# Kernel tuning notes

Measured on AMD Instinct MI355X. Metric: run time of the kernel, lower is better.

Reference implementation:

```python
import jax, jax.numpy as jnp
import numpy as np

D_MODEL, D_STATE, DT_RANK = 1024, 16, 64
BATCH, SEQLEN = 2, 4096

def setup_inputs() -> dict:
    key = jax.random.key(0)
    ks = jax.random.split(key, 6)
    x = jax.random.normal(ks[0], (BATCH, SEQLEN, D_MODEL), dtype=jnp.float32)
    # A = arange(1..N) repeated per channel; A_log = log(A)
    A = jnp.tile(jnp.arange(1, D_STATE + 1, dtype=jnp.float32)[None, :], (D_MODEL, 1))
    A_log = jnp.log(A)
    D_param = jnp.ones((D_MODEL,), dtype=jnp.float32)
    dt_init_std = DT_RANK ** -0.5
    dt_proj_w = jax.random.uniform(ks[1], (D_MODEL, DT_RANK), minval=-dt_init_std, maxval=dt_init_std, dtype=jnp.float32)
    dt = jnp.exp(jax.random.uniform(ks[2], (D_MODEL,)) * (np.log(0.1) - np.log(0.001)) + np.log(0.001))
    dt_proj_b = dt + jnp.log(-jnp.expm1(-dt))
    x_to_dtBC_w = jax.random.normal(ks[3], (DT_RANK + 2 * D_STATE, D_MODEL), dtype=jnp.float32) * (D_MODEL ** -0.5)
    return {"x": x, "A_log": A_log, "D_param": D_param, "dt_proj_w": dt_proj_w, "dt_proj_b": dt_proj_b, "x_to_dtBC_w": x_to_dtBC_w}

def reference(x, A_log, D_param, dt_proj_w, dt_proj_b, x_to_dtBC_w):
    # x: (B,L,D)
    dtBC = jnp.einsum('bld,ed->ble', x, x_to_dtBC_w)            # (B,L,dt_rank+2N)
    dt_in = dtBC[..., :DT_RANK]
    B_in = dtBC[..., DT_RANK:DT_RANK + D_STATE]                  # (B,L,N)
    C_in = dtBC[..., DT_RANK + D_STATE:]                         # (B,L,N)
    dt = jax.nn.softplus(jnp.einsum('blr,dr->bld', dt_in, dt_proj_w) + dt_proj_b)  # (B,L,D)
    A = -jnp.exp(A_log)                                          # (D,N)
    dA = jnp.exp(dt[..., None] * A[None, None])                  # (B,L,D,N)
    dB = dt[..., None] * B_in[:, :, None, :]                     # (B,L,D,N)
    dBx = dB * x[..., None]                                      # (B,L,D,N)

    def step(h, inputs):
        dA_t, dBx_t, C_t = inputs                                # (B,D,N),(B,D,N),(B,N)
        h = dA_t * h + dBx_t
        y_t = jnp.einsum('bdn,bn->bd', h, C_t)
        return h, y_t

    h0 = jnp.zeros((x.shape[0], D_MODEL, D_STATE), dtype=x.dtype)
    xs = (jnp.swapaxes(dA, 0, 1), jnp.swapaxes(dBx, 0, 1), jnp.swapaxes(C_in, 0, 1))
    _, ys = jax.lax.scan(step, h0, xs)                           # (L,B,D)
    y = jnp.swapaxes(ys, 0, 1) + x * D_param[None, None, :]
    return y
```

## Files before the change

kernel.cpp:

```cpp
#include <hip/hip_runtime.h>

#define D_MODEL 1024
#define D_STATE 16
#define DT_RANK 64
#define BATCH 2
#define SEQLEN 4096
#define NROWS (BATCH * SEQLEN)
#define E_DIM (DT_RANK + 2 * D_STATE)
#define CH 32
#define NCH (SEQLEN / CH)

__global__ __launch_bounds__(256)
void k_trans(const float* __restrict__ Wx, const float* __restrict__ W2,
             float* __restrict__ WT, float* __restrict__ W2T) {
  const int bid = blockIdx.x;
  if (bid < 384) {
    const int idx = bid * 256 + threadIdx.x;
    const int k = idx / E_DIM;
    const int e = idx - k * E_DIM;
    WT[idx] = Wx[(size_t)e * D_MODEL + k];
  } else {
    const int idx = (bid - 384) * 256 + threadIdx.x;
    const int r = idx >> 10;
    const int d = idx & 1023;
    W2T[idx] = W2[(size_t)d * DT_RANK + r];
  }
}

#define G1_BM 64
#define KSPLIT 8
#define KSEG (D_MODEL / KSPLIT)

__global__ __launch_bounds__(128)
void k_gemm1(const float* __restrict__ x, const float* __restrict__ WT,
             float* __restrict__ parts) {
  __shared__ float sX[64 * 65];
  const int tid = threadIdx.x;
  const int lane = tid & 63;
  const int e0 = __builtin_amdgcn_readfirstlane((tid >> 6) * 48);
  const int m0 = blockIdx.x * G1_BM;
  const int ks0 = blockIdx.y * KSEG;

  float acc[48];
  #pragma unroll
  for (int j = 0; j < 48; ++j) acc[j] = 0.f;

  for (int kk = 0; kk < KSEG; kk += 64) {
    __syncthreads();
    #pragma unroll
    for (int s = 0; s < 8; ++s) {
      const int f = s * 128 + tid;
      const int r = f >> 4;
      const int k4 = f & 15;
      const float4 v = *reinterpret_cast<const float4*>(
          &x[(size_t)(m0 + r) * D_MODEL + ks0 + kk + k4 * 4]);
      sX[(k4 * 4 + 0) * 65 + r] = v.x;
      sX[(k4 * 4 + 1) * 65 + r] = v.y;
      sX[(k4 * 4 + 2) * 65 + r] = v.z;
      sX[(k4 * 4 + 3) * 65 + r] = v.w;
    }
    __syncthreads();
    #pragma unroll 4
    for (int k = 0; k < 64; ++k) {
      const float xv = sX[k * 65 + lane];
      const float* wrow = WT + (size_t)(ks0 + kk + k) * E_DIM + e0;
      #pragma unroll
      for (int q = 0; q < 12; ++q) {
        const float4 w = *reinterpret_cast<const float4*>(wrow + 4 * q);
        acc[4 * q + 0] = fmaf(xv, w.x, acc[4 * q + 0]);
        acc[4 * q + 1] = fmaf(xv, w.y, acc[4 * q + 1]);
        acc[4 * q + 2] = fmaf(xv, w.z, acc[4 * q + 2]);
        acc[4 * q + 3] = fmaf(xv, w.w, acc[4 * q + 3]);
      }
    }
  }
  float* op = parts + (size_t)blockIdx.y * (NROWS * E_DIM)
            + (size_t)(m0 + lane) * E_DIM + e0;
  #pragma unroll
  for (int q = 0; q < 12; ++q)
    *reinterpret_cast<float4*>(op + 4 * q) =
        make_float4(acc[4 * q + 0], acc[4 * q + 1], acc[4 * q + 2], acc[4 * q + 3]);
}

__global__ __launch_bounds__(256)
void k_reduce(const float* __restrict__ parts, float* __restrict__ dtBC) {
  const int i = blockIdx.x * 256 + threadIdx.x;
  const float4* p = reinterpret_cast<const float4*>(parts);
  float4 a = p[i];
  #pragma unroll
  for (int s = 1; s < KSPLIT; ++s) {
    const float4 b = p[(size_t)s * (NROWS * E_DIM / 4) + i];
    a.x += b.x; a.y += b.y; a.z += b.z; a.w += b.w;
  }
  reinterpret_cast<float4*>(dtBC)[i] = a;
}

#define G2_ROWS 16

__global__ __launch_bounds__(256)
void k_dt(const float* __restrict__ dtBC, const float* __restrict__ W2T,
          const float* __restrict__ b2, float* __restrict__ dt) {
  const int d = blockIdx.x * 256 + threadIdx.x;
  const int m0 = blockIdx.y * G2_ROWS;
  const float bias = b2[d];
  float acc[G2_ROWS];
  #pragma unroll
  for (int i = 0; i < G2_ROWS; ++i) acc[i] = bias;

  for (int r = 0; r < DT_RANK; ++r) {
    const float w = W2T[(size_t)r * D_MODEL + d];
    #pragma unroll
    for (int i = 0; i < G2_ROWS; ++i)
      acc[i] = fmaf(dtBC[(size_t)(m0 + i) * E_DIM + r], w, acc[i]);
  }
  #pragma unroll
  for (int i = 0; i < G2_ROWS; ++i) {
    const float a = acc[i];
    const float sp = (a > 15.f) ? a : __logf(1.f + __expf(a));
    dt[(size_t)(m0 + i) * D_MODEL + d] = sp;
  }
}

__global__ __launch_bounds__(256)
void k_scanA(const float* __restrict__ dt, const float* __restrict__ x,
             const float* __restrict__ dtBC, const float* __restrict__ A_log,
             float* __restrict__ P, float* __restrict__ U) {
  const int d = blockIdx.x * 256 + threadIdx.x;
  const int c = blockIdx.y;
  const int b = blockIdx.z;
  const int t0 = c * CH;

  __shared__ float sB[CH][D_STATE];
  for (int idx = threadIdx.x; idx < CH * D_STATE; idx += 256) {
    const int t = idx >> 4, n = idx & 15;
    sB[t][n] = dtBC[(size_t)(b * SEQLEN + t0 + t) * E_DIM + DT_RANK + n];
  }
  __syncthreads();

  float Ar[D_STATE];
  #pragma unroll
  for (int q = 0; q < 4; ++q) {
    const float4 v = *reinterpret_cast<const float4*>(
        &A_log[(size_t)d * D_STATE + q * 4]);
    Ar[q * 4 + 0] = -__expf(v.x); Ar[q * 4 + 1] = -__expf(v.y);
    Ar[q * 4 + 2] = -__expf(v.z); Ar[q * 4 + 3] = -__expf(v.w);
  }

  float Pr[D_STATE], Ur[D_STATE];
  #pragma unroll
  for (int n = 0; n < D_STATE; ++n) { Pr[n] = 1.f; Ur[n] = 0.f; }

  const float* dtp = dt + (size_t)(b * SEQLEN + t0) * D_MODEL + d;
  const float* xp  = x  + (size_t)(b * SEQLEN + t0) * D_MODEL + d;

  float dtv = dtp[0];
  float xv  = xp[0];
  for (int t = 0; t < CH; ++t) {
    float dtn = 0.f, xn = 0.f;
    if (t + 1 < CH) {
      dtn = dtp[(size_t)(t + 1) * D_MODEL];
      xn  = xp[(size_t)(t + 1) * D_MODEL];
    }
    const float z = dtv * xv;
    #pragma unroll
    for (int n = 0; n < D_STATE; ++n) {
      const float e = __expf(dtv * Ar[n]);
      Ur[n] = fmaf(e, Ur[n], z * sB[t][n]);
      Pr[n] *= e;
    }
    dtv = dtn; xv = xn;
  }
  const size_t base = (size_t)(b * NCH + c) * (D_STATE * D_MODEL) + d;
  #pragma unroll
  for (int n = 0; n < D_STATE; ++n) {
    P[base + (size_t)n * D_MODEL] = Pr[n];
    U[base + (size_t)n * D_MODEL] = Ur[n];
  }
}

__global__ __launch_bounds__(256)
void k_scanB(const float* __restrict__ P, const float* __restrict__ U,
             float* __restrict__ hst) {
  const int idx = blockIdx.x * 256 + threadIdx.x;
  const int b = idx >> 14;
  const int nd = idx & 16383;
  float h = 0.f;
  for (int c = 0; c < NCH; ++c) {
    const size_t off = (size_t)(b * NCH + c) * (D_STATE * D_MODEL) + nd;
    hst[off] = h;
    h = fmaf(P[off], h, U[off]);
  }
}

__global__ __launch_bounds__(256)
void k_scanC(const float* __restrict__ dt, const float* __restrict__ x,
             const float* __restrict__ dtBC, const float* __restrict__ A_log,
             const float* __restrict__ Dp, const float* __restrict__ hst,
             float* __restrict__ y) {
  const int d = blockIdx.x * 256 + threadIdx.x;
  const int c = blockIdx.y;
  const int b = blockIdx.z;
  const int t0 = c * CH;

  __shared__ float sBC[CH][2 * D_STATE];
  for (int idx = threadIdx.x; idx < CH * 2 * D_STATE; idx += 256) {
    const int t = idx >> 5, j = idx & 31;
    sBC[t][j] = dtBC[(size_t)(b * SEQLEN + t0 + t) * E_DIM + DT_RANK + j];
  }
  __syncthreads();

  float Ar[D_STATE];
  #pragma unroll
  for (int q = 0; q < 4; ++q) {
    const float4 v = *reinterpret_cast<const float4*>(
        &A_log[(size_t)d * D_STATE + q * 4]);
    Ar[q * 4 + 0] = -__expf(v.x); Ar[q * 4 + 1] = -__expf(v.y);
    Ar[q * 4 + 2] = -__expf(v.z); Ar[q * 4 + 3] = -__expf(v.w);
  }
  const float Dv = Dp[d];

  float h[D_STATE];
  const size_t hbase = (size_t)(b * NCH + c) * (D_STATE * D_MODEL) + d;
  #pragma unroll
  for (int n = 0; n < D_STATE; ++n) h[n] = hst[hbase + (size_t)n * D_MODEL];

  const float* dtp = dt + (size_t)(b * SEQLEN + t0) * D_MODEL + d;
  const float* xp  = x  + (size_t)(b * SEQLEN + t0) * D_MODEL + d;
  float* yp        = y  + (size_t)(b * SEQLEN + t0) * D_MODEL + d;

  float dtv = dtp[0];
  float xv  = xp[0];
  for (int t = 0; t < CH; ++t) {
    float dtn = 0.f, xn = 0.f;
    if (t + 1 < CH) {
      dtn = dtp[(size_t)(t + 1) * D_MODEL];
      xn  = xp[(size_t)(t + 1) * D_MODEL];
    }
    const float z = dtv * xv;
    float acc = 0.f;
    #pragma unroll
    for (int n = 0; n < D_STATE; ++n) {
      const float e = __expf(dtv * Ar[n]);
      h[n] = fmaf(e, h[n], z * sBC[t][n]);
      acc = fmaf(h[n], sBC[t][D_STATE + n], acc);
    }
    yp[(size_t)t * D_MODEL] = fmaf(xv, Dv, acc);
    dtv = dtn; xv = xn;
  }
}

extern "C" void kernel_launch(void* const* d_in, const int* in_sizes, int n_in,
                              void* d_out, int out_size, void* d_ws, size_t ws_size,
                              hipStream_t stream) {
  const float* x     = (const float*)d_in[0];
  const float* A_log = (const float*)d_in[1];
  const float* Dp    = (const float*)d_in[2];
  const float* W2    = (const float*)d_in[3];
  const float* b2    = (const float*)d_in[4];
  const float* Wx    = (const float*)d_in[5];
  float* out = (float*)d_out;

  float* ws = (float*)d_ws;
  float* dtBC  = ws;
  float* dtbuf = ws +   786432;
  float* P     = ws +  9175040;
  float* U     = ws + 13369344;
  float* hst   = ws + 17563648;
  float* parts = P;
  float* WT    = hst;
  float* W2T   = hst + 98304;

  hipLaunchKernelGGL(k_trans, dim3(640), dim3(256), 0, stream, Wx, W2, WT, W2T);
  hipLaunchKernelGGL(k_gemm1, dim3(NROWS / G1_BM, KSPLIT), dim3(128), 0,
                     stream, x, WT, parts);
  hipLaunchKernelGGL(k_reduce, dim3(NROWS * E_DIM / 4 / 256), dim3(256), 0,
                     stream, parts, dtBC);
  hipLaunchKernelGGL(k_dt, dim3(D_MODEL / 256, NROWS / G2_ROWS), dim3(256), 0,
                     stream, dtBC, W2T, b2, dtbuf);
  hipLaunchKernelGGL(k_scanA, dim3(D_MODEL / 256, NCH, BATCH), dim3(256),
                     0, stream, dtbuf, x, dtBC, A_log, P, U);
  hipLaunchKernelGGL(k_scanB, dim3((BATCH * D_STATE * D_MODEL) / 256),
                     dim3(256), 0, stream, P, U, hst);
  hipLaunchKernelGGL(k_scanC, dim3(D_MODEL / 256, NCH, BATCH), dim3(256),
                     0, stream, dtbuf, x, dtBC, A_log, Dp, hst, out);
}
```

Measured before the change: 235.3 us.

## Replace split-K FP32 projection GEMM with bf16 MFMA kernel, drop reduce pass

Converts the x_to_dtBC weight to bf16 in the prep kernel and rewrites the first projection GEMM to use 16x16x32 bf16 MFMA instructions, converting x to bf16 on the fly. Each 64-thread block computes 16 rows over the full K dimension, which removes the split-K partial buffers and the separate reduction kernel. The cost is reduced precision on the dt/B/C projections, and small one-wave blocks that read x straight from global memory without LDS staging.

```diff
diff --git a/kernel.cpp b/kernel.cpp
--- a/kernel.cpp
+++ b/kernel.cpp
@@ -6,19 +6,23 @@
 #define BATCH 2
 #define SEQLEN 4096
 #define NROWS (BATCH * SEQLEN)
-#define E_DIM (DT_RANK + 2 * D_STATE)
+#define E_DIM 96
 #define CH 32
 #define NCH (SEQLEN / CH)
 
-__global__ __launch_bounds__(256)
-void k_trans(const float* __restrict__ Wx, const float* __restrict__ W2,
-             float* __restrict__ WT, float* __restrict__ W2T) {
+typedef short bf16x8 __attribute__((ext_vector_type(8)));
+typedef float f32x4 __attribute__((ext_vector_type(4)));
+
+__global__ __launch_bounds__(256)
+void k_prep(const float* __restrict__ Wx, const float* __restrict__ W2,
+            unsigned short* __restrict__ Wxbf, float* __restrict__ W2T) {
   const int bid = blockIdx.x;
   if (bid < 384) {
     const int idx = bid * 256 + threadIdx.x;
-    const int k = idx / E_DIM;
-    const int e = idx - k * E_DIM;
-    WT[idx] = Wx[(size_t)e * D_MODEL + k];
+    const float f = Wx[idx];
+    unsigned int u = __float_as_uint(f);
+    u = (u + 0x7fffu + ((u >> 16) & 1u)) >> 16;
+    Wxbf[idx] = (unsigned short)u;
   } else {
     const int idx = (bid - 384) * 256 + threadIdx.x;
     const int r = idx >> 10;
@@ -27,72 +31,43 @@
   }
 }
 
-#define G1_BM 64
-#define KSPLIT 8
-#define KSEG (D_MODEL / KSPLIT)
-
-__global__ __launch_bounds__(128)
-void k_gemm1(const float* __restrict__ x, const float* __restrict__ WT,
-             float* __restrict__ parts) {
-  __shared__ float sX[64 * 65];
-  const int tid = threadIdx.x;
-  const int lane = tid & 63;
-  const int e0 = __builtin_amdgcn_readfirstlane((tid >> 6) * 48);
-  const int m0 = blockIdx.x * G1_BM;
-  const int ks0 = blockIdx.y * KSEG;
-
-  float acc[48];
-  #pragma unroll
-  for (int j = 0; j < 48; ++j) acc[j] = 0.f;
-
-  for (int kk = 0; kk < KSEG; kk += 64) {
-    __syncthreads();
-    #pragma unroll
-    for (int s = 0; s < 8; ++s) {
-      const int f = s * 128 + tid;
-      const int r = f >> 4;
-      const int k4 = f & 15;
-      const float4 v = *reinterpret_cast<const float4*>(
-          &x[(size_t)(m0 + r) * D_MODEL + ks0 + kk + k4 * 4]);
-      sX[(k4 * 4 + 0) * 65 + r] = v.x;
-      sX[(k4 * 4 + 1) * 65 + r] = v.y;
-      sX[(k4 * 4 + 2) * 65 + r] = v.z;
-      sX[(k4 * 4 + 3) * 65 + r] = v.w;
-    }
-    __syncthreads();
-    #pragma unroll 4
-    for (int k = 0; k < 64; ++k) {
-      const float xv = sX[k * 65 + lane];
-      const float* wrow = WT + (size_t)(ks0 + kk + k) * E_DIM + e0;
-      #pragma unroll
-      for (int q = 0; q < 12; ++q) {
-        const float4 w = *reinterpret_cast<const float4*>(wrow + 4 * q);
-        acc[4 * q + 0] = fmaf(xv, w.x, acc[4 * q + 0]);
-        acc[4 * q + 1] = fmaf(xv, w.y, acc[4 * q + 1]);
-        acc[4 * q + 2] = fmaf(xv, w.z, acc[4 * q + 2]);
-        acc[4 * q + 3] = fmaf(xv, w.w, acc[4 * q + 3]);
-      }
-    }
-  }
-  float* op = parts + (size_t)blockIdx.y * (NROWS * E_DIM)
-            + (size_t)(m0 + lane) * E_DIM + e0;
-  #pragma unroll
-  for (int q = 0; q < 12; ++q)
-    *reinterpret_cast<float4*>(op + 4 * q) =
-        make_float4(acc[4 * q + 0], acc[4 * q + 1], acc[4 * q + 2], acc[4 * q + 3]);
-}
-
-__global__ __launch_bounds__(256)
-void k_reduce(const float* __restrict__ parts, float* __restrict__ dtBC) {
-  const int i = blockIdx.x * 256 + threadIdx.x;
-  const float4* p = reinterpret_cast<const float4*>(parts);
-  float4 a = p[i];
-  #pragma unroll
-  for (int s = 1; s < KSPLIT; ++s) {
-    const float4 b = p[(size_t)s * (NROWS * E_DIM / 4) + i];
-    a.x += b.x; a.y += b.y; a.z += b.z; a.w += b.w;
-  }
-  reinterpret_cast<float4*>(dtBC)[i] = a;
+__global__ __launch_bounds__(64)
+void k_gemm1(const float* __restrict__ x, const unsigned short* __restrict__ Wxbf,
+             float* __restrict__ dtBC) {
+  const int lane = threadIdx.x;
+  const int m0 = blockIdx.x * 16;
+  const int r = lane & 15;
+  const int kq = lane >> 4;
+
+  f32x4 acc[6];
+  #pragma unroll
+  for (int j = 0; j < 6; ++j) acc[j] = (f32x4){0.f, 0.f, 0.f, 0.f};
+
+  const float* xrow = x + (size_t)(m0 + r) * D_MODEL + kq * 8;
+  const unsigned short* wbase = Wxbf + (size_t)r * D_MODEL + kq * 8;
+
+  #pragma unroll 2
+  for (int k0 = 0; k0 < D_MODEL; k0 += 32) {
+    const float4 a0 = *reinterpret_cast<const float4*>(xrow + k0);
+    const float4 a1 = *reinterpret_cast<const float4*>(xrow + k0 + 4);
+    union { unsigned int u[4]; bf16x8 v; } ua;
+    asm("v_cvt_pk_bf16_f32 %0, %1, %2" : "=v"(ua.u[0]) : "v"(a0.x), "v"(a0.y));
+    asm("v_cvt_pk_bf16_f32 %0, %1, %2" : "=v"(ua.u[1]) : "v"(a0.z), "v"(a0.w));
+    asm("v_cvt_pk_bf16_f32 %0, %1, %2" : "=v"(ua.u[2]) : "v"(a1.x), "v"(a1.y));
+    asm("v_cvt_pk_bf16_f32 %0, %1, %2" : "=v"(ua.u[3]) : "v"(a1.z), "v"(a1.w));
+    const bf16x8 af = ua.v;
+    #pragma unroll
+    for (int j = 0; j < 6; ++j) {
+      const bf16x8 bf = *reinterpret_cast<const bf16x8*>(
+          wbase + (size_t)j * 16 * D_MODEL + k0);
+      acc[j] = __builtin_amdgcn_mfma_f32_16x16x32_bf16(af, bf, acc[j], 0, 0, 0);
+    }
+  }
+  #pragma unroll
+  for (int j = 0; j < 6; ++j)
+    #pragma unroll
+    for (int i = 0; i < 4; ++i)
+      dtBC[(size_t)(m0 + kq * 4 + i) * E_DIM + j * 16 + r] = acc[j][i];
 }
 
 #define G2_ROWS 16
@@ -266,15 +241,12 @@
   float* P     = ws +  9175040;
   float* U     = ws + 13369344;
   float* hst   = ws + 17563648;
-  float* parts = P;
-  float* WT    = hst;
-  float* W2T   = hst + 98304;
-
-  hipLaunchKernelGGL(k_trans, dim3(640), dim3(256), 0, stream, Wx, W2, WT, W2T);
-  hipLaunchKernelGGL(k_gemm1, dim3(NROWS / G1_BM, KSPLIT), dim3(128), 0,
-                     stream, x, WT, parts);
-  hipLaunchKernelGGL(k_reduce, dim3(NROWS * E_DIM / 4 / 256), dim3(256), 0,
-                     stream, parts, dtBC);
+  unsigned short* Wxbf = (unsigned short*)hst;
+  float* W2T           = hst + 49152;
+
+  hipLaunchKernelGGL(k_prep, dim3(640), dim3(256), 0, stream, Wx, W2, Wxbf, W2T);
+  hipLaunchKernelGGL(k_gemm1, dim3(NROWS / 16), dim3(64), 0, stream,
+                     x, Wxbf, dtBC);
   hipLaunchKernelGGL(k_dt, dim3(D_MODEL / 256, NROWS / G2_ROWS), dim3(256), 0,
                      stream, dtBC, W2T, b2, dtbuf);
   hipLaunchKernelGGL(k_scanA, dim3(D_MODEL / 256, NCH, BATCH), dim3(256),
```

New measurement: 217.5 us. -7.6%, faster.
